# Optimization experiments

Measured on AMD Instinct MI355X. Metric: run time of the kernel, lower is better.

Reference implementation:

```python
import jax, jax.numpy as jnp
import numpy as np

N_NODES = 100000
N_EDGES = 1600000


def setup_inputs() -> dict:
    key = jax.random.key(0)
    ks = jax.random.split(key, 10)
    inp = {
        "inputs": jax.random.normal(ks[0], (N_NODES, 32), dtype=jnp.float32),
        "src": jax.random.randint(ks[1], (N_EDGES,), 0, N_NODES, dtype=jnp.int64)
            if jax.config.jax_enable_x64 else jax.random.randint(ks[1], (N_EDGES,), 0, N_NODES).astype(jnp.int32),
        "dst": jax.random.randint(ks[2], (N_EDGES,), 0, N_NODES).astype(jnp.int32),
        "W_self1": jax.random.normal(ks[3], (32, 32), dtype=jnp.float32) * 0.1,
        "W_neigh1": jax.random.normal(ks[4], (32, 32), dtype=jnp.float32) * 0.1,
        "b1": jnp.zeros((32,), dtype=jnp.float32),
        "W_self2": jax.random.normal(ks[5], (32, 32), dtype=jnp.float32) * 0.1,
        "W_neigh2": jax.random.normal(ks[6], (32, 32), dtype=jnp.float32) * 0.1,
        "b2": jnp.zeros((32,), dtype=jnp.float32),
        "W_self3": jax.random.normal(ks[7], (32, 16), dtype=jnp.float32) * 0.1,
        "W_neigh3": jax.random.normal(ks[8], (32, 16), dtype=jnp.float32) * 0.1,
        "b3": jnp.zeros((16,), dtype=jnp.float32),
    }
    inp["src"] = inp["src"].astype(jnp.int32)
    return inp


def _sage_mean(h, src, dst, deg_inv, W_self, W_neigh, b):
    # gather src features, sum into dst, divide by in-degree -> mean aggregation
    msg_sum = jax.ops.segment_sum(h[src], dst, num_segments=N_NODES)  # [N, d]
    h_neigh = msg_sum * deg_inv[:, None]
    return h @ W_self + h_neigh @ W_neigh + b


def reference(inputs, src, dst, W_self1, W_neigh1, b1, W_self2, W_neigh2, b2,
              W_self3, W_neigh3, b3):
    ones = jnp.ones((src.shape[0],), dtype=inputs.dtype)
    deg = jax.ops.segment_sum(ones, dst, num_segments=N_NODES)
    deg_inv = jnp.where(deg > 0, 1.0 / jnp.maximum(deg, 1.0), 0.0)

    h = jax.nn.sigmoid(_sage_mean(inputs, src, dst, deg_inv, W_self1, W_neigh1, b1))
    h = jax.nn.sigmoid(_sage_mean(h, src, dst, deg_inv, W_self2, W_neigh2, b2))
    h = jax.nn.sigmoid(_sage_mean(h, src, dst, deg_inv, W_self3, W_neigh3, b3))
    return h
```

## Files before the change

### kernel.cpp

```cpp
#include <hip/hip_runtime.h>

#define NN 100000
#define NE 1600000
#define DPAD 16

typedef float f4 __attribute__((ext_vector_type(4)));
typedef unsigned short us4 __attribute__((ext_vector_type(4)));

__device__ __forceinline__ float bf2f(unsigned short v) {
    return __builtin_bit_cast(float, ((unsigned)v) << 16);
}
__device__ __forceinline__ unsigned short f2bf(float f) {
    unsigned u = __builtin_bit_cast(unsigned, f);
    return (unsigned short)((u + 0x7FFF + ((u >> 16) & 1)) >> 16);
}

__global__ __launch_bounds__(256) void k_build1(const int* __restrict__ dst,
                                                int* __restrict__ deg,
                                                unsigned short* __restrict__ rank,
                                                const f4* __restrict__ in4,
                                                unsigned* __restrict__ q4) {
    int e = blockIdx.x * 256 + threadIdx.x;
    int d = dst[e];
    rank[e] = (unsigned short)atomicAdd(&deg[d * DPAD], 1);
    if (e < NN * 32 / 4) {
        f4 v = in4[e];
        unsigned w = 0;
#pragma unroll
        for (int c = 0; c < 4; ++c) {
            float y = fminf(fmaxf(v[c] * (255.0f / 11.0f) + 128.0f, 0.0f), 255.0f);
            w |= ((unsigned)(int)y) << (8 * c);
        }
        q4[e] = w;
    }
}

__global__ void k_scan1(const int* __restrict__ deg, int* __restrict__ offs,
                        int* __restrict__ bsums) {
    __shared__ int ts[256];
    int b = blockIdx.x, t = threadIdx.x;
    int base = b * 1024 + t * 4;
    int v[4];
    int s = 0;
#pragma unroll
    for (int i = 0; i < 4; ++i) {
        int idx = base + i;
        v[i] = (idx < NN) ? deg[idx * DPAD] : 0;
        s += v[i];
    }
    ts[t] = s;
    __syncthreads();
    for (int off = 1; off < 256; off <<= 1) {
        int x = (t >= off) ? ts[t - off] : 0;
        __syncthreads();
        ts[t] += x;
        __syncthreads();
    }
    int excl = ts[t] - s;
#pragma unroll
    for (int i = 0; i < 4; ++i) {
        int idx = base + i;
        if (idx < NN) offs[idx] = excl;
        excl += v[i];
    }
    if (t == 255) bsums[b] = ts[255];
}

__global__ void k_scan2(int* __restrict__ bsums, int nb) {
    int lane = threadIdx.x;
    int v0 = (lane < nb) ? bsums[lane] : 0;
    int v1 = (64 + lane < nb) ? bsums[64 + lane] : 0;
    int s0 = v0, s1 = v1;
    for (int o = 1; o < 64; o <<= 1) {
        int t0 = __shfl_up(s0, o, 64);
        int t1 = __shfl_up(s1, o, 64);
        if (lane >= o) { s0 += t0; s1 += t1; }
    }
    int tot0 = __shfl(s0, 63, 64);
    if (lane < nb) bsums[lane] = s0 - v0;
    if (64 + lane < nb) bsums[64 + lane] = tot0 + s1 - v1;
}

__global__ void k_scan3(int* __restrict__ offs, const int* __restrict__ bsums) {
    int i = blockIdx.x * blockDim.x + threadIdx.x;
    if (i < NN) {
        offs[i] += bsums[i >> 10];
        if (i == 0) offs[NN] = NE;
    }
}

__global__ __launch_bounds__(256) void k_scatter(const int* __restrict__ src,
                                                 const int* __restrict__ dst,
                                                 const unsigned short* __restrict__ rank,
                                                 const int* __restrict__ offs,
                                                 int* __restrict__ ssrc) {
    int e = blockIdx.x * 256 + threadIdx.x;
    ssrc[offs[dst[e]] + (int)rank[e]] = src[e];
}

__global__ __launch_bounds__(256) void k_agg(const unsigned* __restrict__ qt,
                                             const int* __restrict__ offs,
                                             const int* __restrict__ ssrc,
                                             float scale, float bcorr,
                                             unsigned short* __restrict__ hn) {
    const int lane = threadIdx.x & 63;
    const int h = lane >> 5;
    const int l5 = lane & 31;
    const int fq = l5 & 7;
    const int slot = l5 >> 3;
    const int stride = gridDim.x * 8;

    for (int node = blockIdx.x * 8 + (threadIdx.x >> 6) * 2 + h; node < NN;
         node += stride) {
        const int e0 = offs[node], e1 = offs[node + 1];
        unsigned a0 = 0, a1 = 0;
        int e = e0 + slot;
        for (; e + 12 < e1; e += 16) {
            unsigned w0 = qt[ssrc[e] * 8 + fq];
            unsigned w1 = qt[ssrc[e + 4] * 8 + fq];
            unsigned w2 = qt[ssrc[e + 8] * 8 + fq];
            unsigned w3 = qt[ssrc[e + 12] * 8 + fq];
            a0 += (w0 & 0x00ff00ffu) + (w1 & 0x00ff00ffu) +
                  (w2 & 0x00ff00ffu) + (w3 & 0x00ff00ffu);
            a1 += ((w0 >> 8) & 0x00ff00ffu) + ((w1 >> 8) & 0x00ff00ffu) +
                  ((w2 >> 8) & 0x00ff00ffu) + ((w3 >> 8) & 0x00ff00ffu);
        }
        for (; e < e1; e += 4) {
            unsigned w0 = qt[ssrc[e] * 8 + fq];
            a0 += (w0 & 0x00ff00ffu);
            a1 += ((w0 >> 8) & 0x00ff00ffu);
        }
        a0 += __shfl_xor(a0, 8, 64);
        a1 += __shfl_xor(a1, 8, 64);
        a0 += __shfl_xor(a0, 16, 64);
        a1 += __shfl_xor(a1, 16, 64);
        if (slot == 0) {
            const int dg = e1 - e0;
            const float sc = (dg > 0) ? scale / (float)dg : 0.0f;
            const float bb = (dg > 0) ? bcorr : 0.0f;
            us4 o;
            o[0] = f2bf((float)(a0 & 0xffffu) * sc - bb);
            o[1] = f2bf((float)(a1 & 0xffffu) * sc - bb);
            o[2] = f2bf((float)(a0 >> 16) * sc - bb);
            o[3] = f2bf((float)(a1 >> 16) * sc - bb);
            *(us4*)(hn + node * 32 + fq * 4) = o;
        }
    }
}

template <int OUTF, bool SELF32, bool OUTQ>
__global__ __launch_bounds__(256) void k_mlp(
    const float* __restrict__ hinf, const unsigned char* __restrict__ qself,
    float sscale, const unsigned short* __restrict__ hn,
    const float* __restrict__ Ws, const float* __restrict__ Wn,
    const float* __restrict__ bias,
    float* __restrict__ outf, unsigned char* __restrict__ outq) {
    __shared__ float sWs[32 * OUTF];
    __shared__ float sWn[32 * OUTF];
    __shared__ float sB[OUTF];
    __shared__ float sHs[256];
    __shared__ float sHn[256];
    for (int i = threadIdx.x; i < 32 * OUTF; i += 256) {
        sWs[i] = Ws[i];
        sWn[i] = Wn[i];
    }
    if (threadIdx.x < OUTF) sB[threadIdx.x] = bias[threadIdx.x];

    const int t = threadIdx.x;
    const int n = t >> 5;
    const int jj = t & (OUTF - 1);
    const int stride = gridDim.x * 8;

    for (int base = blockIdx.x * 8; base < NN; base += stride) {
        const int node = base + n;
        float hv;
        if (SELF32) hv = hinf[base * 32 + t];
        else hv = (float)qself[base * 32 + t] * sscale;
        float nv = bf2f(hn[base * 32 + t]);
        __syncthreads();
        sHs[t] = hv;
        sHn[t] = nv;
        __syncthreads();
        float acc = sB[jj];
#pragma unroll 8
        for (int k = 0; k < 32; ++k) {
            acc += sHs[n * 32 + k] * sWs[k * OUTF + jj] +
                   sHn[n * 32 + k] * sWn[k * OUTF + jj];
        }
        if ((t & 31) < OUTF) {
            float s = 1.0f / (1.0f + __expf(-acc));
            if (OUTQ) outq[node * OUTF + jj] = (unsigned char)(int)(s * 255.0f + 0.5f);
            else outf[node * OUTF + jj] = s;
        }
    }
}


extern "C" void kernel_launch(void* const* d_in, const int* in_sizes, int n_in,
                              void* d_out, int out_size, void* d_ws, size_t ws_size,
                              hipStream_t stream) {
    const float* inputs = (const float*)d_in[0];
    const int* src = (const int*)d_in[1];
    const int* dst = (const int*)d_in[2];
    const float* Ws1 = (const float*)d_in[3];
    const float* Wn1 = (const float*)d_in[4];
    const float* b1 = (const float*)d_in[5];
    const float* Ws2 = (const float*)d_in[6];
    const float* Wn2 = (const float*)d_in[7];
    const float* b2 = (const float*)d_in[8];
    const float* Ws3 = (const float*)d_in[9];
    const float* Wn3 = (const float*)d_in[10];
    const float* b3 = (const float*)d_in[11];
    float* out = (float*)d_out;

    int* ws = (int*)d_ws;
    int* deg = ws;
    int* offs = ws + 1600000;
    int* bsums = ws + 1700016;
    int* ssrc = ws + 1700160;
    unsigned short* rank = (unsigned short*)(ws + 3300160);
    unsigned* qA = (unsigned*)(ws + 4100160);
    unsigned* q1 = (unsigned*)(ws + 4900160);
    unsigned* q2 = (unsigned*)(ws + 5700160);
    unsigned short* hn = (unsigned short*)(ws + 6500160);

    hipMemsetAsync(deg, 0, NN * DPAD * sizeof(int), stream);

    k_build1<<<NE / 256, 256, 0, stream>>>(dst, deg, rank, (const f4*)inputs, qA);
    k_scan1<<<98, 256, 0, stream>>>(deg, offs, bsums);
    k_scan2<<<1, 64, 0, stream>>>(bsums, 98);
    k_scan3<<<(NN + 255) / 256, 256, 0, stream>>>(offs, bsums);
    k_scatter<<<NE / 256, 256, 0, stream>>>(src, dst, rank, offs, ssrc);

    k_agg<<<2048, 256, 0, stream>>>(qA, offs, ssrc, 11.0f / 255.0f, 5.5f, hn);
    k_mlp<32, true, true><<<2048, 256, 0, stream>>>(
        inputs, nullptr, 0.0f, hn, Ws1, Wn1, b1, nullptr, (unsigned char*)q1);
    k_agg<<<2048, 256, 0, stream>>>(q1, offs, ssrc, 1.0f / 255.0f, 0.0f, hn);
    k_mlp<32, false, true><<<2048, 256, 0, stream>>>(
        nullptr, (const unsigned char*)q1, 1.0f / 255.0f, hn, Ws2, Wn2, b2,
        nullptr, (unsigned char*)q2);
    k_agg<<<2048, 256, 0, stream>>>(q2, offs, ssrc, 1.0f / 255.0f, 0.0f, hn);
    k_mlp<16, false, false><<<2048, 256, 0, stream>>>(
        nullptr, (const unsigned char*)q2, 1.0f / 255.0f, hn, Ws3, Wn3, b3,
        out, nullptr);
}
```

Measured before the change: 314.4 us.

## Replace global-atomic CSR build with two-pass radix bucket sort by destination

Builds the destination-sorted edge list with a two-level counting sort instead of global atomics. Edges are first histogrammed per 512-node bucket in shared memory, a block-by-bucket count matrix is scanned, and edges are scattered into buckets as packed (low dst bits, src) words. A per-bucket 1024-thread kernel then computes node offsets and places the src indices. This removes 1.6M contended global atomicAdds, the memset and the rank array, but adds an extra pass over the edges and relies on src fitting in 17 bits.

```diff
diff --git a/kernel.cpp b/kernel.cpp
--- a/kernel.cpp
+++ b/kernel.cpp
@@ -2,7 +2,10 @@
 
 #define NN 100000
 #define NE 1600000
-#define DPAD 16
+#define NB 196
+#define SB 512
+#define NBLK 1563
+#define NMAT (NB * NBLK)
 
 typedef float f4 __attribute__((ext_vector_type(4)));
 typedef unsigned short us4 __attribute__((ext_vector_type(4)));
@@ -15,28 +18,40 @@
     return (unsigned short)((u + 0x7FFF + ((u >> 16) & 1)) >> 16);
 }
 
-__global__ __launch_bounds__(256) void k_build1(const int* __restrict__ dst,
-                                                int* __restrict__ deg,
-                                                unsigned short* __restrict__ rank,
-                                                const f4* __restrict__ in4,
-                                                unsigned* __restrict__ q4) {
-    int e = blockIdx.x * 256 + threadIdx.x;
-    int d = dst[e];
-    rank[e] = (unsigned short)atomicAdd(&deg[d * DPAD], 1);
-    if (e < NN * 32 / 4) {
-        f4 v = in4[e];
-        unsigned w = 0;
-#pragma unroll
-        for (int c = 0; c < 4; ++c) {
-            float y = fminf(fmaxf(v[c] * (255.0f / 11.0f) + 128.0f, 0.0f), 255.0f);
-            w |= ((unsigned)(int)y) << (8 * c);
-        }
-        q4[e] = w;
-    }
-}
-
-__global__ void k_scan1(const int* __restrict__ deg, int* __restrict__ offs,
-                        int* __restrict__ bsums) {
+__global__ __launch_bounds__(256) void k_hist(const int* __restrict__ dst,
+                                              int* __restrict__ mat,
+                                              const f4* __restrict__ in4,
+                                              unsigned* __restrict__ q4) {
+    __shared__ int cnt[NB];
+    const int b = blockIdx.x, t = threadIdx.x;
+    if (t < NB) cnt[t] = 0;
+    __syncthreads();
+#pragma unroll
+    for (int i = 0; i < 4; ++i) {
+        int e = b * 1024 + i * 256 + t;
+        if (e < NE) atomicAdd(&cnt[dst[e] >> 9], 1);
+    }
+    __syncthreads();
+    if (t < NB) mat[t * NBLK + b] = cnt[t];
+    const int gid = b * 256 + t;
+#pragma unroll
+    for (int rep = 0; rep < 2; ++rep) {
+        int idx = gid + rep * 400064;
+        if (idx < NN * 32 / 4) {
+            f4 v = in4[idx];
+            unsigned w = 0;
+#pragma unroll
+            for (int c = 0; c < 4; ++c) {
+                float y = fminf(fmaxf(v[c] * (255.0f / 11.0f) + 128.0f, 0.0f), 255.0f);
+                w |= ((unsigned)(int)y) << (8 * c);
+            }
+            q4[idx] = w;
+        }
+    }
+}
+
+__global__ void k_scanA(const int* __restrict__ in, int* __restrict__ out,
+                        int* __restrict__ bsums, int N) {
     __shared__ int ts[256];
     int b = blockIdx.x, t = threadIdx.x;
     int base = b * 1024 + t * 4;
@@ -45,7 +60,7 @@
 #pragma unroll
     for (int i = 0; i < 4; ++i) {
         int idx = base + i;
-        v[i] = (idx < NN) ? deg[idx * DPAD] : 0;
+        v[i] = (idx < N) ? in[idx] : 0;
         s += v[i];
     }
     ts[t] = s;
@@ -60,42 +75,88 @@
 #pragma unroll
     for (int i = 0; i < 4; ++i) {
         int idx = base + i;
-        if (idx < NN) offs[idx] = excl;
+        if (idx < N) out[idx] = excl;
         excl += v[i];
     }
     if (t == 255) bsums[b] = ts[255];
 }
 
-__global__ void k_scan2(int* __restrict__ bsums, int nb) {
-    int lane = threadIdx.x;
-    int v0 = (lane < nb) ? bsums[lane] : 0;
-    int v1 = (64 + lane < nb) ? bsums[64 + lane] : 0;
-    int s0 = v0, s1 = v1;
-    for (int o = 1; o < 64; o <<= 1) {
-        int t0 = __shfl_up(s0, o, 64);
-        int t1 = __shfl_up(s1, o, 64);
-        if (lane >= o) { s0 += t0; s1 += t1; }
-    }
-    int tot0 = __shfl(s0, 63, 64);
-    if (lane < nb) bsums[lane] = s0 - v0;
-    if (64 + lane < nb) bsums[64 + lane] = tot0 + s1 - v1;
-}
-
-__global__ void k_scan3(int* __restrict__ offs, const int* __restrict__ bsums) {
+__global__ void k_scanB(int* __restrict__ bsums, int nb) {
+    __shared__ int ts[512];
+    int t = threadIdx.x;
+    int v = (t < nb) ? bsums[t] : 0;
+    ts[t] = v;
+    __syncthreads();
+    for (int off = 1; off < 512; off <<= 1) {
+        int x = (t >= off) ? ts[t - off] : 0;
+        __syncthreads();
+        ts[t] += x;
+        __syncthreads();
+    }
+    if (t < nb) bsums[t] = ts[t] - v;
+}
+
+__global__ void k_scanC(int* __restrict__ out, const int* __restrict__ bsums, int N) {
     int i = blockIdx.x * blockDim.x + threadIdx.x;
-    if (i < NN) {
-        offs[i] += bsums[i >> 10];
-        if (i == 0) offs[NN] = NE;
-    }
-}
-
-__global__ __launch_bounds__(256) void k_scatter(const int* __restrict__ src,
-                                                 const int* __restrict__ dst,
-                                                 const unsigned short* __restrict__ rank,
-                                                 const int* __restrict__ offs,
-                                                 int* __restrict__ ssrc) {
-    int e = blockIdx.x * 256 + threadIdx.x;
-    ssrc[offs[dst[e]] + (int)rank[e]] = src[e];
+    if (i < N) out[i] += bsums[i >> 10];
+}
+
+__global__ __launch_bounds__(256) void k_scat(const int* __restrict__ src,
+                                              const int* __restrict__ dst,
+                                              const int* __restrict__ matS,
+                                              unsigned* __restrict__ bkt) {
+    __shared__ int lcur[NB];
+    const int b = blockIdx.x, t = threadIdx.x;
+    if (t < NB) lcur[t] = 0;
+    __syncthreads();
+#pragma unroll
+    for (int i = 0; i < 4; ++i) {
+        int e = b * 1024 + i * 256 + t;
+        if (e < NE) {
+            int dv = dst[e];
+            int d = dv >> 9;
+            int r = atomicAdd(&lcur[d], 1);
+            int pos = matS[d * NBLK + b] + r;
+            bkt[pos] = ((unsigned)(dv & 511) << 17) | (unsigned)src[e];
+        }
+    }
+}
+
+__global__ __launch_bounds__(1024) void k_p2(const unsigned* __restrict__ bkt,
+                                             const int* __restrict__ matS,
+                                             int* __restrict__ offs,
+                                             int* __restrict__ ssrc) {
+    __shared__ int ts[SB];
+    __shared__ int pre[SB];
+    __shared__ int cur[SB];
+    const int d = blockIdx.x, t = threadIdx.x;
+    const int start = matS[d * NBLK];
+    const int end = (d == NB - 1) ? NE : matS[(d + 1) * NBLK];
+    if (t < SB) { ts[t] = 0; cur[t] = 0; }
+    __syncthreads();
+    for (int e = start + t; e < end; e += 1024)
+        atomicAdd(&ts[bkt[e] >> 17], 1);
+    __syncthreads();
+    int orig = (t < SB) ? ts[t] : 0;
+    for (int off = 1; off < SB; off <<= 1) {
+        int x = (t >= off && t < SB) ? ts[t - off] : 0;
+        __syncthreads();
+        if (t < SB) ts[t] += x;
+        __syncthreads();
+    }
+    if (t < SB) {
+        pre[t] = ts[t] - orig;
+        int node = d * SB + t;
+        if (node < NN) offs[node] = start + pre[t];
+    }
+    if (d == NB - 1 && t == 0) offs[NN] = NE;
+    __syncthreads();
+    for (int e = start + t; e < end; e += 1024) {
+        unsigned w = bkt[e];
+        int dlow = w >> 17;
+        int r = atomicAdd(&cur[dlow], 1);
+        ssrc[start + pre[dlow] + r] = (int)(w & 0x1FFFFu);
+    }
 }
 
 __global__ __launch_bounds__(256) void k_agg(const unsigned* __restrict__ qt,
@@ -214,23 +275,23 @@
     float* out = (float*)d_out;
 
     int* ws = (int*)d_ws;
-    int* deg = ws;
-    int* offs = ws + 1600000;
-    int* bsums = ws + 1700016;
-    int* ssrc = ws + 1700160;
-    unsigned short* rank = (unsigned short*)(ws + 3300160);
-    unsigned* qA = (unsigned*)(ws + 4100160);
-    unsigned* q1 = (unsigned*)(ws + 4900160);
-    unsigned* q2 = (unsigned*)(ws + 5700160);
-    unsigned short* hn = (unsigned short*)(ws + 6500160);
-
-    hipMemsetAsync(deg, 0, NN * DPAD * sizeof(int), stream);
-
-    k_build1<<<NE / 256, 256, 0, stream>>>(dst, deg, rank, (const f4*)inputs, qA);
-    k_scan1<<<98, 256, 0, stream>>>(deg, offs, bsums);
-    k_scan2<<<1, 64, 0, stream>>>(bsums, 98);
-    k_scan3<<<(NN + 255) / 256, 256, 0, stream>>>(offs, bsums);
-    k_scatter<<<NE / 256, 256, 0, stream>>>(src, dst, rank, offs, ssrc);
+    int* mat = ws;
+    int* matS = ws + 306352;
+    int* bsums = ws + 612704;
+    int* offs = ws + 613216;
+    unsigned* bkt = (unsigned*)(ws + 713232);
+    int* ssrc = ws + 2313232;
+    unsigned* qA = (unsigned*)(ws + 3913232);
+    unsigned* q1 = (unsigned*)(ws + 4713232);
+    unsigned* q2 = (unsigned*)(ws + 5513232);
+    unsigned short* hn = (unsigned short*)(ws + 6313232);
+
+    k_hist<<<NBLK, 256, 0, stream>>>(dst, mat, (const f4*)inputs, qA);
+    k_scanA<<<300, 256, 0, stream>>>(mat, matS, bsums, NMAT);
+    k_scanB<<<1, 512, 0, stream>>>(bsums, 300);
+    k_scanC<<<(NMAT + 255) / 256, 256, 0, stream>>>(matS, bsums, NMAT);
+    k_scat<<<NBLK, 256, 0, stream>>>(src, dst, matS, bkt);
+    k_p2<<<NB, 1024, 0, stream>>>(bkt, matS, offs, ssrc);
 
     k_agg<<<2048, 256, 0, stream>>>(qA, offs, ssrc, 11.0f / 255.0f, 5.5f, hn);
     k_mlp<32, true, true><<<2048, 256, 0, stream>>>(
```

Result: faster. 261.7 us (-16.8%).
